# Kernel optimization log

Measured on AMD Instinct MI355X. Metric: run time of the kernel, lower is better.

Reference implementation:

```python
import jax, jax.numpy as jnp
import numpy as np


def setup_inputs() -> dict:
    key = jax.random.key(0)
    k1, k2, k3, k4 = jax.random.split(key, 4)
    B, Q, D, H = 8, 512, 4096, 1024
    return {
        "query_embeddings": jax.random.normal(k1, (B, Q, H), dtype=jnp.float32),
        "document_embeddings": jax.random.normal(k2, (B, D, H), dtype=jnp.float32),
        "attention_mask": jax.random.randint(k3, (B, D), 0, 2, dtype=jnp.int32),
        "proj_w": jax.random.normal(k4, (H, H), dtype=jnp.float32) * (H ** -0.5),
        "proj_b": jnp.zeros((H,), dtype=jnp.float32),
    }


def reference(query_embeddings, document_embeddings, attention_mask, proj_w, proj_b):
    H = query_embeddings.shape[-1]
    scale = 1.0 / jnp.sqrt(jnp.asarray(H, dtype=query_embeddings.dtype))
    # Linear projection of queries: [B, Q, H]
    q = jnp.einsum("bqh,hk->bqk", query_embeddings, proj_w) + proj_b
    # Scores: [B, Q, D]
    scores = jnp.einsum("bqh,bdh->bqd", q, document_embeddings) * scale
    # Mask: [B, 1, D]; masked positions -> -inf before softmax
    mask = attention_mask[:, None, :] != 0
    scores = jnp.where(mask, scores, -jnp.inf)
    attention_weights = jax.nn.softmax(scores, axis=-1)
    # Weighted sum over docs: [B, Q, H]
    retrieved_docs = jnp.einsum("bqd,bdh->bqh", attention_weights, document_embeddings)
    return (retrieved_docs, attention_weights)
```

## Files before the change

### kernel.cpp

```cpp
#include <hip/hip_runtime.h>

#define BATCH 8
#define QLEN 512
#define DLEN 4096
#define HDIM 1024

typedef __attribute__((ext_vector_type(8))) short bf16x8;
typedef __attribute__((ext_vector_type(4))) float f32x4;
typedef __attribute__((ext_vector_type(4))) short s16x4;

__device__ __forceinline__ short f2bf(float f) {
    union { float f; unsigned u; } x; x.f = f;
    unsigned r = x.u + 0x7fffu + ((x.u >> 16) & 1u);
    return (short)(r >> 16);
}

__device__ __forceinline__ void gload_lds16(const void* g, void* l) {
    __builtin_amdgcn_global_load_lds(
        (const __attribute__((address_space(1))) unsigned int*)g,
        (__attribute__((address_space(3))) unsigned int*)l,
        16, 0, 0);
}

__global__ void cvt_f32_bf16(const float* __restrict__ in, short* __restrict__ out, int n4) {
    int i = blockIdx.x * blockDim.x + threadIdx.x;
    int stride = gridDim.x * blockDim.x;
    for (; i < n4; i += stride) {
        float4 x = ((const float4*)in)[i];
        s16x4 o = { f2bf(x.x), f2bf(x.y), f2bf(x.z), f2bf(x.w) };
        ((s16x4*)out)[i] = o;
    }
}

__global__ void transpose_w(const float* __restrict__ W, short* __restrict__ Wt) {
    __shared__ float t[32][33];
    const int hb = blockIdx.y * 32, kb = blockIdx.x * 32;
    #pragma unroll
    for (int i = 0; i < 4; ++i) {
        int h = threadIdx.y + i * 8;
        t[h][threadIdx.x] = W[(size_t)(hb + h) * HDIM + kb + threadIdx.x];
    }
    __syncthreads();
    #pragma unroll
    for (int i = 0; i < 4; ++i) {
        int k = threadIdx.y + i * 8;
        Wt[(size_t)(kb + k) * HDIM + hb + threadIdx.x] = f2bf(t[threadIdx.x][k]);
    }
}

__global__ void transpose_docs(const short* __restrict__ docsB, short* __restrict__ docsT) {
    __shared__ unsigned t[64][65];
    const int b = blockIdx.z;
    const int h0 = blockIdx.x * 64, d0 = blockIdx.y * 64;
    const int tq = threadIdx.x & 15;
    const int tr = threadIdx.x >> 4;
    #pragma unroll
    for (int i = 0; i < 4; ++i) {
        int d = tr + i * 16;
        s16x4 v = *(const s16x4*)(docsB + ((size_t)b * DLEN + d0 + d) * HDIM + h0 + tq * 4);
        t[d][tq * 4 + 0] = (unsigned short)v[0];
        t[d][tq * 4 + 1] = (unsigned short)v[1];
        t[d][tq * 4 + 2] = (unsigned short)v[2];
        t[d][tq * 4 + 3] = (unsigned short)v[3];
    }
    __syncthreads();
    #pragma unroll
    for (int i = 0; i < 4; ++i) {
        int h = tr + i * 16;
        s16x4 o = { (short)t[tq * 4 + 0][h], (short)t[tq * 4 + 1][h],
                    (short)t[tq * 4 + 2][h], (short)t[tq * 4 + 3][h] };
        *(s16x4*)(docsT + ((size_t)b * HDIM + h0 + h) * DLEN + d0 + tq * 4) = o;
    }
}

#define BM 128
#define BN 128
#define BK 64

template<int EPI>
__global__ void gemm_bt(const short* __restrict__ A, const short* __restrict__ B,
                        void* __restrict__ Cv, const float* __restrict__ bias,
                        float scale, int N, int Kstride, int Kloop, int kOffStep,
                        int sx, int sxy,
                        long long aB, long long bB, long long cB) {
    __shared__ short As[BM * BK];
    __shared__ short Bs[BN * BK];
    const int tid  = threadIdx.x;
    const int lane = tid & 63;
    const int wv   = tid >> 6;
    const int wr   = wv >> 1, wc = wv & 1;

    const int wg = (blockIdx.x & 7) * (gridDim.x >> 3) + (blockIdx.x >> 3);
    const int bx = wg & ((1 << sx) - 1);
    const int by = (wg >> sx) & ((1 << (sxy - sx)) - 1);
    const int z  = wg >> sxy;

    const size_t rowBase = (size_t)by * BM;
    const size_t colBase = (size_t)bx * BN;
    const int bb = z & 7;
    const int kOff = (z >> 3) * kOffStep;
    const short* Ag = A + (size_t)bb * aB + kOff;
    const short* Bg = B + (size_t)bb * bB + kOff;

    f32x4 acc[4][4];
    #pragma unroll
    for (int m = 0; m < 4; ++m)
        #pragma unroll
        for (int n = 0; n < 4; ++n)
            acc[m][n] = (f32x4){0.f, 0.f, 0.f, 0.f};

    const short* aSrc[4]; const short* bSrc[4]; short* aDst[4]; short* bDst[4];
    #pragma unroll
    for (int i = 0; i < 4; ++i) {
        const int c = tid + 256 * i;
        const int r = c >> 3, cc = c & 7;
        const int gk = (cc ^ (r & 7)) << 3;
        aSrc[i] = Ag + (rowBase + r) * (size_t)Kstride + gk;
        bSrc[i] = Bg + (colBase + r) * (size_t)Kstride + gk;
        aDst[i] = As + c * 8;
        bDst[i] = Bs + c * 8;
    }
    const int lr = lane & 15;
    const int lk = (lane >> 4) << 3;

    for (int kt = 0; kt < Kloop; kt += BK) {
        #pragma unroll
        for (int i = 0; i < 4; ++i) gload_lds16(aSrc[i] + kt, aDst[i]);
        #pragma unroll
        for (int i = 0; i < 4; ++i) gload_lds16(bSrc[i] + kt, bDst[i]);
        __syncthreads();

        #pragma unroll
        for (int kk = 0; kk < 2; ++kk) {
            const int chunkL = (kk * 32 + lk) >> 3;
            bf16x8 af[4], bfr[4];
            #pragma unroll
            for (int m = 0; m < 4; ++m) {
                const int row = wr * 64 + m * 16 + lr;
                af[m] = *(const bf16x8*)(As + row * BK + ((chunkL ^ (row & 7)) << 3));
            }
            #pragma unroll
            for (int n = 0; n < 4; ++n) {
                const int row = wc * 64 + n * 16 + lr;
                bfr[n] = *(const bf16x8*)(Bs + row * BK + ((chunkL ^ (row & 7)) << 3));
            }
            #pragma unroll
            for (int m = 0; m < 4; ++m)
                #pragma unroll
                for (int n = 0; n < 4; ++n)
                    acc[m][n] = __builtin_amdgcn_mfma_f32_16x16x32_bf16(af[m], bfr[n], acc[m][n], 0, 0, 0);
        }
        __syncthreads();
    }

    const int orow = (lane >> 4) << 2;
    const int ocol = lane & 15;
    #pragma unroll
    for (int n = 0; n < 4; ++n) {
        const size_t col = colBase + wc * 64 + n * 16 + ocol;
        const float bv = (EPI == 0) ? bias[col] : 0.f;
        #pragma unroll
        for (int m = 0; m < 4; ++m) {
            const size_t rbase = rowBase + wr * 64 + m * 16 + orow;
            #pragma unroll
            for (int j = 0; j < 4; ++j) {
                const float v = acc[m][n][j];
                const size_t off = (size_t)z * cB + (rbase + j) * (size_t)N + col;
                if (EPI == 0)      ((short*)Cv)[off] = f2bf(v + bv);
                else if (EPI == 1) ((float*)Cv)[off] = v * scale;
                else               ((float*)Cv)[off] = v;
            }
        }
    }
}

__global__ void reduce4(const float* __restrict__ p, float* __restrict__ out, int n4) {
    int i = blockIdx.x * blockDim.x + threadIdx.x;
    const int stride = gridDim.x * blockDim.x;
    const float4* p4 = (const float4*)p;
    float4* o4 = (float4*)out;
    for (; i < n4; i += stride) {
        float4 a = p4[i];
        float4 b = p4[i + 1048576];
        float4 c = p4[i + 2097152];
        float4 d = p4[i + 3145728];
        float4 r;
        r.x = a.x + b.x + c.x + d.x;
        r.y = a.y + b.y + c.y + d.y;
        r.z = a.z + b.z + c.z + d.z;
        r.w = a.w + b.w + c.w + d.w;
        o4[i] = r;
    }
}

__global__ void softmax_rows(const float* __restrict__ scores, const int* __restrict__ mask,
                             float* __restrict__ attnF, short* __restrict__ attnB) {
    const int row = blockIdx.x;
    const int b   = row >> 9;
    const int tid = threadIdx.x;
    const int lane = tid & 63;
    const int wv = tid >> 6;
    const float4* S  = (const float4*)(scores + (size_t)row * DLEN);
    const int4*   Mk = (const int4*)(mask + (size_t)b * DLEN);
    __shared__ float red[8];

    float v[16];
    float mx = -INFINITY;
    #pragma unroll
    for (int i = 0; i < 4; ++i) {
        float4 s = S[i * 256 + tid];
        int4   m = Mk[i * 256 + tid];
        v[i * 4 + 0] = m.x ? s.x : -INFINITY;
        v[i * 4 + 1] = m.y ? s.y : -INFINITY;
        v[i * 4 + 2] = m.z ? s.z : -INFINITY;
        v[i * 4 + 3] = m.w ? s.w : -INFINITY;
        #pragma unroll
        for (int c = 0; c < 4; ++c) mx = fmaxf(mx, v[i * 4 + c]);
    }
    #pragma unroll
    for (int o = 32; o > 0; o >>= 1) mx = fmaxf(mx, __shfl_xor(mx, o));
    if (lane == 0) red[wv] = mx;
    __syncthreads();
    mx = fmaxf(fmaxf(red[0], red[1]), fmaxf(red[2], red[3]));

    float sum = 0.f;
    #pragma unroll
    for (int i = 0; i < 16; ++i) {
        float e = __expf(v[i] - mx);
        v[i] = e;
        sum += e;
    }
    #pragma unroll
    for (int o = 32; o > 0; o >>= 1) sum += __shfl_xor(sum, o);
    __syncthreads();
    if (lane == 0) red[4 + wv] = sum;
    __syncthreads();
    sum = red[4] + red[5] + red[6] + red[7];
    const float inv = 1.0f / sum;

    float4* OF = (float4*)(attnF + (size_t)row * DLEN);
    s16x4*  OB = (s16x4*)(attnB + (size_t)row * DLEN);
    #pragma unroll
    for (int i = 0; i < 4; ++i) {
        float4 w;
        w.x = v[i * 4 + 0] * inv;
        w.y = v[i * 4 + 1] * inv;
        w.z = v[i * 4 + 2] * inv;
        w.w = v[i * 4 + 3] * inv;
        OF[i * 256 + tid] = w;
        s16x4 o = { f2bf(w.x), f2bf(w.y), f2bf(w.z), f2bf(w.w) };
        OB[i * 256 + tid] = o;
    }
}

extern "C" void kernel_launch(void* const* d_in, const int* in_sizes, int n_in,
                              void* d_out, int out_size, void* d_ws, size_t ws_size,
                              hipStream_t stream) {
    const float* qe   = (const float*)d_in[0];
    const float* docs = (const float*)d_in[1];
    const int*   mask = (const int*)d_in[2];
    const float* pw   = (const float*)d_in[3];
    const float* pb   = (const float*)d_in[4];

    float* outRet  = (float*)d_out;
    float* outAttn = outRet + (size_t)BATCH * QLEN * HDIM;

    char* ws = (char*)d_ws;
    short* qeB   = (short*)(ws + 0);
    short* wt    = (short*)(ws + 8388608);
    short* qpB   = (short*)(ws + 10485760);
    short* docsB = (short*)(ws + 18874368);
    short* docsT = (short*)(ws + 85983232);
    float* scor  = (float*)(ws + 153092096);
    short* attnB = (short*)(ws + 220200960);

    cvt_f32_bf16<<<dim3(1024), dim3(256), 0, stream>>>(qe, qeB, (BATCH * QLEN * HDIM) / 4);
    cvt_f32_bf16<<<dim3(2048), dim3(256), 0, stream>>>(docs, docsB, (BATCH * DLEN * HDIM) / 4);
    transpose_w<<<dim3(32, 32), dim3(32, 8), 0, stream>>>(pw, wt);
    transpose_docs<<<dim3(HDIM / 64, DLEN / 64, BATCH), dim3(256), 0, stream>>>(docsB, docsT);

    gemm_bt<0><<<dim3(256), dim3(256), 0, stream>>>(
        qeB, wt, (void*)qpB, pb, 1.f, HDIM, HDIM, HDIM, 0, 3, 8,
        0LL, 0LL, 0LL);

    gemm_bt<1><<<dim3(1024), dim3(256), 0, stream>>>(
        qpB, docsB, (void*)scor, nullptr, 0.03125f, DLEN, HDIM, HDIM, 0, 5, 7,
        (long long)QLEN * HDIM, (long long)DLEN * HDIM, (long long)QLEN * DLEN);

    softmax_rows<<<dim3(BATCH * QLEN), dim3(256), 0, stream>>>(scor, mask, outAttn, attnB);

    gemm_bt<2><<<dim3(1024), dim3(256), 0, stream>>>(
        attnB, docsT, (void*)scor, nullptr, 1.f, HDIM, DLEN, DLEN / 4, DLEN / 4, 3, 5,
        (long long)QLEN * DLEN, (long long)HDIM * DLEN, (long long)QLEN * HDIM);

    reduce4<<<dim3(2048), dim3(256), 0, stream>>>(scor, outRet, (BATCH * QLEN * HDIM) / 4);
}
```

Measured before the change: 414.4 us.

## Double-buffer GEMM LDS tiles with async prefetch two stages ahead

Doubles the LDS A/B tiles in the bf16 GEMM and issues global-to-LDS loads for tile t+2 while tile t's MFMAs run, using explicit vmcnt/lgkmcnt waits and raw s_barrier instead of __syncthreads. All fragments for a tile are loaded into registers before the barrier, so the buffer can be refilled during compute. The aim is to hide global load latency behind matrix math. It also raises wave priority around the MFMA block. In exchange it doubles LDS use, which may lower occupancy, raises register pressure, and relies on correct hand-placed wait counts.

After: 714.5 us. +72.4%, slower.

```diff
diff --git a/kernel.cpp b/kernel.cpp
--- a/kernel.cpp
+++ b/kernel.cpp
@@ -21,6 +21,9 @@
         (__attribute__((address_space(3))) unsigned int*)l,
         16, 0, 0);
 }
+
+#define WAIT_VMCNT(n) asm volatile("s_waitcnt vmcnt(" #n ")" ::: "memory")
+#define WAIT_LGKM0    asm volatile("s_waitcnt lgkmcnt(0)" ::: "memory")
 
 __global__ void cvt_f32_bf16(const float* __restrict__ in, short* __restrict__ out, int n4) {
     int i = blockIdx.x * blockDim.x + threadIdx.x;
@@ -76,6 +79,7 @@
 #define BM 128
 #define BN 128
 #define BK 64
+#define TILE_SH (BM * BK)
 
 template<int EPI>
 __global__ void gemm_bt(const short* __restrict__ A, const short* __restrict__ B,
@@ -83,8 +87,8 @@
                         float scale, int N, int Kstride, int Kloop, int kOffStep,
                         int sx, int sxy,
                         long long aB, long long bB, long long cB) {
-    __shared__ short As[BM * BK];
-    __shared__ short Bs[BN * BK];
+    __shared__ short As[2 * TILE_SH];
+    __shared__ short Bs[2 * TILE_SH];
     const int tid  = threadIdx.x;
     const int lane = tid & 63;
     const int wv   = tid >> 6;
@@ -109,7 +113,7 @@
         for (int n = 0; n < 4; ++n)
             acc[m][n] = (f32x4){0.f, 0.f, 0.f, 0.f};
 
-    const short* aSrc[4]; const short* bSrc[4]; short* aDst[4]; short* bDst[4];
+    const short* aSrc[4]; const short* bSrc[4]; int dOff[4];
     #pragma unroll
     for (int i = 0; i < 4; ++i) {
         const int c = tid + 256 * i;
@@ -117,40 +121,71 @@
         const int gk = (cc ^ (r & 7)) << 3;
         aSrc[i] = Ag + (rowBase + r) * (size_t)Kstride + gk;
         bSrc[i] = Bg + (colBase + r) * (size_t)Kstride + gk;
-        aDst[i] = As + c * 8;
-        bDst[i] = Bs + c * 8;
+        dOff[i] = c * 8;
     }
     const int lr = lane & 15;
     const int lk = (lane >> 4) << 3;
 
-    for (int kt = 0; kt < Kloop; kt += BK) {
-        #pragma unroll
-        for (int i = 0; i < 4; ++i) gload_lds16(aSrc[i] + kt, aDst[i]);
-        #pragma unroll
-        for (int i = 0; i < 4; ++i) gload_lds16(bSrc[i] + kt, bDst[i]);
-        __syncthreads();
-
+    const int nt = Kloop / BK;
+
+    #pragma unroll
+    for (int i = 0; i < 4; ++i) gload_lds16(aSrc[i], As + dOff[i]);
+    #pragma unroll
+    for (int i = 0; i < 4; ++i) gload_lds16(bSrc[i], Bs + dOff[i]);
+    #pragma unroll
+    for (int i = 0; i < 4; ++i) gload_lds16(aSrc[i] + BK, As + TILE_SH + dOff[i]);
+    #pragma unroll
+    for (int i = 0; i < 4; ++i) gload_lds16(bSrc[i] + BK, Bs + TILE_SH + dOff[i]);
+    WAIT_VMCNT(8);
+    __builtin_amdgcn_s_barrier();
+
+    for (int t = 0; t < nt; ++t) {
+        const int c = t & 1;
+        const short* Ab = As + c * TILE_SH;
+        const short* Bb = Bs + c * TILE_SH;
+
+        bf16x8 af[2][4], bfr[2][4];
         #pragma unroll
         for (int kk = 0; kk < 2; ++kk) {
             const int chunkL = (kk * 32 + lk) >> 3;
-            bf16x8 af[4], bfr[4];
             #pragma unroll
             for (int m = 0; m < 4; ++m) {
                 const int row = wr * 64 + m * 16 + lr;
-                af[m] = *(const bf16x8*)(As + row * BK + ((chunkL ^ (row & 7)) << 3));
+                af[kk][m] = *(const bf16x8*)(Ab + row * BK + ((chunkL ^ (row & 7)) << 3));
             }
             #pragma unroll
             for (int n = 0; n < 4; ++n) {
                 const int row = wc * 64 + n * 16 + lr;
-                bfr[n] = *(const bf16x8*)(Bs + row * BK + ((chunkL ^ (row & 7)) << 3));
+                bfr[kk][n] = *(const bf16x8*)(Bb + row * BK + ((chunkL ^ (row & 7)) << 3));
             }
+        }
+        WAIT_LGKM0;
+        __builtin_amdgcn_sched_barrier(0);
+        __builtin_amdgcn_s_barrier();
+
+        if (t + 2 < nt) {
+            const int kt2 = (t + 2) * BK;
+            #pragma unroll
+            for (int i = 0; i < 4; ++i) gload_lds16(aSrc[i] + kt2, As + c * TILE_SH + dOff[i]);
+            #pragma unroll
+            for (int i = 0; i < 4; ++i) gload_lds16(bSrc[i] + kt2, Bs + c * TILE_SH + dOff[i]);
+        }
+
+        __builtin_amdgcn_s_setprio(1);
+        #pragma unroll
+        for (int kk = 0; kk < 2; ++kk)
             #pragma unroll
             for (int m = 0; m < 4; ++m)
                 #pragma unroll
                 for (int n = 0; n < 4; ++n)
-                    acc[m][n] = __builtin_amdgcn_mfma_f32_16x16x32_bf16(af[m], bfr[n], acc[m][n], 0, 0, 0);
+                    acc[m][n] = __builtin_amdgcn_mfma_f32_16x16x32_bf16(af[kk][m], bfr[kk][n], acc[m][n], 0, 0, 0);
+        __builtin_amdgcn_s_setprio(0);
+
+        if (t + 1 < nt) {
+            if (t + 2 < nt) { WAIT_VMCNT(8); }
+            else           { WAIT_VMCNT(0); }
+            __builtin_amdgcn_s_barrier();
         }
-        __syncthreads();
     }
 
     const int orow = (lane >> 4) << 2;
```

## Double-buffer LDS tiles in GEMM to overlap global loads with MFMA

Applied to the files above, without the earlier changes.

Splits the shared-memory A and B tiles into two buffers and issues the async global-to-LDS loads for the next K tile before computing on the current one, leaving one barrier per iteration. This is meant to hide global memory latency behind the MFMA work. It doubles LDS use per block (64 KB), which may lower occupancy. The single barrier relies on global_load_lds completion ordering at that barrier.

After: 421.4 us. About the same (+1.7%).

```diff
diff --git a/kernel.cpp b/kernel.cpp
--- a/kernel.cpp
+++ b/kernel.cpp
@@ -76,6 +76,7 @@
 #define BM 128
 #define BN 128
 #define BK 64
+#define TILE_SH (BM * BK)
 
 template<int EPI>
 __global__ void gemm_bt(const short* __restrict__ A, const short* __restrict__ B,
@@ -83,8 +84,8 @@
                         float scale, int N, int Kstride, int Kloop, int kOffStep,
                         int sx, int sxy,
                         long long aB, long long bB, long long cB) {
-    __shared__ short As[BM * BK];
-    __shared__ short Bs[BN * BK];
+    __shared__ short As[2 * TILE_SH];
+    __shared__ short Bs[2 * TILE_SH];
     const int tid  = threadIdx.x;
     const int lane = tid & 63;
     const int wv   = tid >> 6;
@@ -109,7 +110,7 @@
         for (int n = 0; n < 4; ++n)
             acc[m][n] = (f32x4){0.f, 0.f, 0.f, 0.f};
 
-    const short* aSrc[4]; const short* bSrc[4]; short* aDst[4]; short* bDst[4];
+    const short* aSrc[4]; const short* bSrc[4]; int dOff[4];
     #pragma unroll
     for (int i = 0; i < 4; ++i) {
         const int c = tid + 256 * i;
@@ -117,19 +118,32 @@
         const int gk = (cc ^ (r & 7)) << 3;
         aSrc[i] = Ag + (rowBase + r) * (size_t)Kstride + gk;
         bSrc[i] = Bg + (colBase + r) * (size_t)Kstride + gk;
-        aDst[i] = As + c * 8;
-        bDst[i] = Bs + c * 8;
+        dOff[i] = c * 8;
     }
     const int lr = lane & 15;
     const int lk = (lane >> 4) << 3;
 
-    for (int kt = 0; kt < Kloop; kt += BK) {
-        #pragma unroll
-        for (int i = 0; i < 4; ++i) gload_lds16(aSrc[i] + kt, aDst[i]);
-        #pragma unroll
-        for (int i = 0; i < 4; ++i) gload_lds16(bSrc[i] + kt, bDst[i]);
-        __syncthreads();
-
+    const int nt = Kloop / BK;
+
+    #pragma unroll
+    for (int i = 0; i < 4; ++i) gload_lds16(aSrc[i], As + dOff[i]);
+    #pragma unroll
+    for (int i = 0; i < 4; ++i) gload_lds16(bSrc[i], Bs + dOff[i]);
+    __syncthreads();
+
+    int cur = 0;
+    for (int t = 0; t < nt; ++t) {
+        if (t + 1 < nt) {
+            const int kt = (t + 1) * BK;
+            const int o = (cur ^ 1) * TILE_SH;
+            #pragma unroll
+            for (int i = 0; i < 4; ++i) gload_lds16(aSrc[i] + kt, As + o + dOff[i]);
+            #pragma unroll
+            for (int i = 0; i < 4; ++i) gload_lds16(bSrc[i] + kt, Bs + o + dOff[i]);
+        }
+
+        const short* Ab = As + cur * TILE_SH;
+        const short* Bb = Bs + cur * TILE_SH;
         #pragma unroll
         for (int kk = 0; kk < 2; ++kk) {
             const int chunkL = (kk * 32 + lk) >> 3;
@@ -137,12 +151,12 @@
             #pragma unroll
             for (int m = 0; m < 4; ++m) {
                 const int row = wr * 64 + m * 16 + lr;
-                af[m] = *(const bf16x8*)(As + row * BK + ((chunkL ^ (row & 7)) << 3));
+                af[m] = *(const bf16x8*)(Ab + row * BK + ((chunkL ^ (row & 7)) << 3));
             }
             #pragma unroll
             for (int n = 0; n < 4; ++n) {
                 const int row = wc * 64 + n * 16 + lr;
-                bfr[n] = *(const bf16x8*)(Bs + row * BK + ((chunkL ^ (row & 7)) << 3));
+                bfr[n] = *(const bf16x8*)(Bb + row * BK + ((chunkL ^ (row & 7)) << 3));
             }
             #pragma unroll
             for (int m = 0; m < 4; ++m)
@@ -151,6 +165,7 @@
                     acc[m][n] = __builtin_amdgcn_mfma_f32_16x16x32_bf16(af[m], bfr[n], acc[m][n], 0, 0, 0);
         }
         __syncthreads();
+        cur ^= 1;
     }
 
     const int orow = (lane >> 4) << 2;
```
